# Performance work log

Hardware: AMD Instinct MI355X
Metric: run time of the kernel (lower is better)

Reference implementation:

```python
import jax, jax.numpy as jnp
import numpy as np

B, N, F, H, E = 2, 20000, 128, 1, 640000
C = F  # out_channels per head (concat=False -> mean over heads)
NEG_SLOPE = 0.2


def setup_inputs() -> dict:
    key = jax.random.key(0)
    k = jax.random.split(key, 6)
    x = jax.random.normal(k[0], (B, N, F), dtype=jnp.float32)
    edge_index = jax.random.randint(k[1], (2, E), 0, N, dtype=jnp.int64)
    s = 1.0 / np.sqrt(F)
    W = jax.random.normal(k[2], (H * C, F), dtype=jnp.float32) * s      # PyG Linear weight
    att_src = jax.random.normal(k[3], (H, C), dtype=jnp.float32) * s
    att_dst = jax.random.normal(k[4], (H, C), dtype=jnp.float32) * s
    bias = jnp.zeros((C,), dtype=jnp.float32)
    return {"x": x, "edge_index": edge_index, "W": W,
            "att_src": att_src, "att_dst": att_dst, "bias": bias}


def _gat_single(x, src, dst, W, att_src, att_dst, bias):
    # x: [N, F]; src/dst: [E'] (self-loops already appended)
    h = (x @ W.T).reshape(N, H, C)                      # [N, H, C]
    a_src = jnp.einsum('nhc,hc->nh', h, att_src)        # [N, H]
    a_dst = jnp.einsum('nhc,hc->nh', h, att_dst)        # [N, H]
    logits = jax.nn.leaky_relu(a_src[src] + a_dst[dst], NEG_SLOPE)  # [E', H]
    # edge-softmax over incoming edges of each dst node
    seg_max = jax.ops.segment_max(logits, dst, num_segments=N)      # [N, H]
    e = jnp.exp(logits - seg_max[dst])
    denom = jax.ops.segment_sum(e, dst, num_segments=N)             # [N, H]
    alpha = e / denom[dst]                                          # [E', H]
    msg = h[src] * alpha[:, :, None]                                # [E', H, C]
    out = jax.ops.segment_sum(msg, dst, num_segments=N)             # [N, H, C]
    return out.mean(axis=1) + bias                                  # [N, C]


def reference(x, edge_index, W, att_src, att_dst, bias):
    # PyG GATConv default: add self-loops
    loops = jnp.arange(N, dtype=edge_index.dtype)
    src = jnp.concatenate([edge_index[0], loops])
    dst = jnp.concatenate([edge_index[1], loops])
    f = lambda xb: _gat_single(xb, src, dst, W, att_src, att_dst, bias)
    return jax.vmap(f)(x)  # [B, N, F]
```

## Files before the change

### kernel.cpp

```cpp
#include <hip/hip_runtime.h>
#include <hip/hip_bf16.h>
#include <math.h>

#define BB    2
#define NN    20000
#define FF    128
#define EE    640000
#define NBIN  157
#define NBLK  625
#define SEGW  32
#define BSLOTS (NBLK * SEGW)
#define RECCAP 5120
#define GEMM_BLOCKS 625
#define SLOPE 0.2f

typedef __attribute__((ext_vector_type(8))) short bf16x8;
typedef __attribute__((ext_vector_type(4))) float f32x4;

static __device__ __forceinline__ ushort f2bf(float f) {
    unsigned u = __float_as_uint(f);
    u += 0x7fffu + ((u >> 16) & 1u);
    return (ushort)(u >> 16);
}
static __device__ __forceinline__ float bf2f(unsigned hw) {
    return __uint_as_float(hw << 16);
}
static __device__ __forceinline__ float bflo(unsigned q) {
    return __uint_as_float(q << 16);
}
static __device__ __forceinline__ float bfhi(unsigned q) {
    return __uint_as_float(q & 0xffff0000u);
}

__global__ __launch_bounds__(256) void fused_kernel(
    const float* __restrict__ x, const float* __restrict__ W,
    const float* __restrict__ att_src, const float* __restrict__ att_dst,
    const int* __restrict__ ei,
    unsigned* __restrict__ hbu, float* __restrict__ as2, float* __restrict__ ad2,
    ushort* __restrict__ cnts, unsigned* __restrict__ binbuf)
{
    __shared__ ushort XL[64 * 128];
    __shared__ ushort WL[128 * 128];
    const int tid = threadIdx.x;

    if (blockIdx.x >= GEMM_BLOCKS) {
        const int b2 = blockIdx.x - GEMM_BLOCKS;
        const int e0 = b2 * 1024;
        int* hcnt = (int*)XL;
        int* hofs = hcnt + 160;
        int* hcur = hofs + 160;
        int* scan = hcur + 160;
        unsigned* stage = (unsigned*)WL;

        for (int i = tid; i < NBIN; i += 256) { hcnt[i] = 0; hcur[i] = 0; }
        __syncthreads();

        int bin[4]; unsigned word[4];
        #pragma unroll
        for (int k = 0; k < 4; ++k) {
            int e = e0 + k * 256 + tid;
            int s = ei[e], d = ei[EE + e];
            bool ok = ((unsigned)s < NN) && ((unsigned)d < NN);
            bin[k] = ok ? (d >> 7) : -1;
            word[k] = ((unsigned)(d & 127) << 15) | (unsigned)(s & 0x7fff);
            if (ok) atomicAdd(&hcnt[bin[k]], 1);
        }
        __syncthreads();
        scan[tid] = (tid < NBIN) ? hcnt[tid] : 0;
        __syncthreads();
        #pragma unroll
        for (int o = 1; o < 256; o <<= 1) {
            int v = (tid >= o) ? scan[tid - o] : 0;
            __syncthreads();
            scan[tid] += v;
            __syncthreads();
        }
        if (tid < NBIN) hofs[tid] = scan[tid] - hcnt[tid];
        if (tid == 0) hofs[NBIN] = scan[NBIN - 1];
        if (tid < NBIN) cnts[b2 * NBIN + tid] = (ushort)min(hcnt[tid], SEGW);
        __syncthreads();
        #pragma unroll
        for (int k = 0; k < 4; ++k) {
            if (bin[k] >= 0) {
                int slot = atomicAdd(&hcur[bin[k]], 1);
                stage[hofs[bin[k]] + slot] = word[k];
            }
        }
        __syncthreads();
        const int total = hofs[NBIN];
        for (int i = tid; i < total; i += 256) {
            int lo = 0, hi = NBIN;
            while (hi - lo > 1) { int mid = (lo + hi) >> 1; if (hofs[mid] <= i) lo = mid; else hi = mid; }
            int j = i - hofs[lo];
            if (j < SEGW)
                binbuf[(size_t)lo * BSLOTS + b2 * SEGW + j] = stage[i];
        }
        return;
    }

    const int r0 = blockIdx.x * 64;
    {
        const float4* xg = (const float4*)(x + (size_t)r0 * 128);
        #pragma unroll
        for (int i = 0; i < 8; ++i) {
            int idx = tid + i * 256;
            int r = idx >> 5, k = (idx & 31) * 4;
            float4 v = xg[idx];
            ushort4 p = { f2bf(v.x), f2bf(v.y), f2bf(v.z), f2bf(v.w) };
            unsigned byte = ((unsigned)r << 8) + ((unsigned)k << 1);
            byte ^= (unsigned)(r & 7) << 4;
            *(ushort4*)((char*)XL + byte) = p;
        }
    }
    {
        const float4* wg = (const float4*)W;
        #pragma unroll
        for (int i = 0; i < 16; ++i) {
            int idx = tid + i * 256;
            int c = idx >> 5, k = (idx & 31) * 4;
            float4 v = wg[idx];
            ushort4 p = { f2bf(v.x), f2bf(v.y), f2bf(v.z), f2bf(v.w) };
            unsigned byte = ((unsigned)c << 8) + ((unsigned)k << 1);
            byte ^= (unsigned)(c & 7) << 4;
            *(ushort4*)((char*)WL + byte) = p;
        }
    }
    __syncthreads();

    const int wid = tid >> 6, lane = tid & 63;
    const int l15 = lane & 15, lg = lane >> 4;
    f32x4 acc[8];
    #pragma unroll
    for (int i = 0; i < 8; ++i) acc[i] = (f32x4){0.f, 0.f, 0.f, 0.f};

    const int arow = wid * 16 + l15;
    #pragma unroll
    for (int kt = 0; kt < 4; ++kt) {
        unsigned abyte = ((unsigned)arow << 8) + (unsigned)(kt * 64 + lg * 16);
        abyte ^= (unsigned)(arow & 7) << 4;
        bf16x8 af = *(const bf16x8*)((const char*)XL + abyte);
        #pragma unroll
        for (int ct = 0; ct < 8; ++ct) {
            int c = ct * 16 + l15;
            unsigned bbyte = ((unsigned)c << 8) + (unsigned)(kt * 64 + lg * 16);
            bbyte ^= (unsigned)(c & 7) << 4;
            bf16x8 bfr = *(const bf16x8*)((const char*)WL + bbyte);
            acc[ct] = __builtin_amdgcn_mfma_f32_16x16x32_bf16(af, bfr, acc[ct], 0, 0, 0);
        }
    }

    float ps0=0,ps1=0,ps2=0,ps3=0, pd0=0,pd1=0,pd2=0,pd3=0;
    #pragma unroll
    for (int ct = 0; ct < 8; ++ct) {
        int c = ct * 16 + l15;
        float as_ = att_src[c], ad_ = att_dst[c];
        ps0 += acc[ct][0]*as_; pd0 += acc[ct][0]*ad_;
        ps1 += acc[ct][1]*as_; pd1 += acc[ct][1]*ad_;
        ps2 += acc[ct][2]*as_; pd2 += acc[ct][2]*ad_;
        ps3 += acc[ct][3]*as_; pd3 += acc[ct][3]*ad_;
    }
    #pragma unroll
    for (int o = 1; o < 16; o <<= 1) {
        ps0 += __shfl_xor(ps0, o, 64); pd0 += __shfl_xor(pd0, o, 64);
        ps1 += __shfl_xor(ps1, o, 64); pd1 += __shfl_xor(pd1, o, 64);
        ps2 += __shfl_xor(ps2, o, 64); pd2 += __shfl_xor(pd2, o, 64);
        ps3 += __shfl_xor(ps3, o, 64); pd3 += __shfl_xor(pd3, o, 64);
    }
    if (l15 == 0) {
        int rb = r0 + wid * 16 + lg * 4;
        #pragma unroll
        for (int q = 0; q < 4; ++q) {
            int r = rb + q;
            int b = (r >= NN);
            int n = r - b * NN;
            float ps = q==0?ps0 : q==1?ps1 : q==2?ps2 : ps3;
            float pd = q==0?pd0 : q==1?pd1 : q==2?pd2 : pd3;
            as2[n * 2 + b] = ps;
            ad2[n * 2 + b] = pd;
        }
    }

    __syncthreads();
    ushort* hl = (ushort*)WL;
    {
        int rb = wid * 16 + lg * 4;
        #pragma unroll
        for (int ct = 0; ct < 8; ++ct) {
            int c = ct * 16 + l15;
            hl[(rb+0) * 128 + c] = f2bf(acc[ct][0]);
            hl[(rb+1) * 128 + c] = f2bf(acc[ct][1]);
            hl[(rb+2) * 128 + c] = f2bf(acc[ct][2]);
            hl[(rb+3) * 128 + c] = f2bf(acc[ct][3]);
        }
    }
    __syncthreads();
    {
        const unsigned* hs = (const unsigned*)hl;
        #pragma unroll
        for (int i = 0; i < 16; ++i) {
            int idx = tid + i * 256;
            int row = idx >> 6, p = idx & 63;
            int r = r0 + row;
            int b = (r >= NN);
            int n = r - b * NN;
            hbu[(size_t)n * 128 + p * 2 + b] = hs[row * 64 + p];
        }
    }
}

__global__ __launch_bounds__(1024) void sort_kernel(
    const ushort* __restrict__ cnts, const unsigned* __restrict__ binbuf,
    const float2* __restrict__ as2, const float2* __restrict__ ad2,
    uint2* __restrict__ rec, int* __restrict__ nodeStart,
    int* __restrict__ nodeCnt)
{
    __shared__ ushort cb[NBLK];
    __shared__ int ncnt[128];
    __shared__ int scan[128];
    __shared__ int nofs[128];
    __shared__ int ncur[128];
    const int b = blockIdx.x;
    const int tid = threadIdx.x;
    const unsigned* src = binbuf + (size_t)b * BSLOTS;

    for (int i = tid; i < NBLK; i += 1024) cb[i] = cnts[i * NBIN + b];
    if (tid < 128) {
        int n = b * 128 + tid;
        int self = (n < NN) ? 1 : 0;
        ncnt[tid] = self;
        ncur[tid] = self;
    }
    __syncthreads();
    for (int idx = tid; idx < BSLOTS; idx += 1024) {
        if ((idx & (SEGW - 1)) < cb[idx >> 5])
            atomicAdd(&ncnt[src[idx] >> 15], 1);
    }
    __syncthreads();
    if (tid < 128) scan[tid] = ncnt[tid];
    __syncthreads();
    #pragma unroll
    for (int o = 1; o < 128; o <<= 1) {
        int v = 0;
        if (tid < 128 && tid >= o) v = scan[tid - o];
        __syncthreads();
        if (tid < 128) scan[tid] += v;
        __syncthreads();
    }
    if (tid < 128) {
        nofs[tid] = scan[tid] - ncnt[tid];
        int n = b * 128 + tid;
        if (n < NN) {
            nodeStart[n] = b * RECCAP + nofs[tid];
            nodeCnt[n]   = ncnt[tid];
            float2 av = as2[n];
            float2 dv = ad2[n];
            float l0 = av.x + dv.x; l0 = l0 > 0.f ? l0 : SLOPE * l0;
            float l1 = av.y + dv.y; l1 = l1 > 0.f ? l1 : SLOPE * l1;
            int pos = nofs[tid];
            if (pos < RECCAP) {
                uint2 r = { (unsigned)n | ((unsigned)f2bf(__expf(l0)) << 16),
                            (unsigned)f2bf(__expf(l1)) };
                rec[(size_t)b * RECCAP + pos] = r;
            }
        }
    }
    __syncthreads();
    for (int idx = tid; idx < BSLOTS; idx += 1024) {
        if ((idx & (SEGW - 1)) < cb[idx >> 5]) {
            unsigned w = src[idx];
            int dl = w >> 15;
            int s  = w & 0x7fff;
            int d  = b * 128 + dl;
            float2 av = as2[s];
            float2 dv = ad2[d];
            float l0 = av.x + dv.x; l0 = l0 > 0.f ? l0 : SLOPE * l0;
            float l1 = av.y + dv.y; l1 = l1 > 0.f ? l1 : SLOPE * l1;
            int slot = atomicAdd(&ncur[dl], 1);
            int pos = nofs[dl] + slot;
            if (pos < RECCAP) {
                uint2 r = { (unsigned)s | ((unsigned)f2bf(__expf(l0)) << 16),
                            (unsigned)f2bf(__expf(l1)) };
                rec[(size_t)b * RECCAP + pos] = r;
            }
        }
    }
}

__global__ __launch_bounds__(256) void gather_kernel(
    const uint2* __restrict__ h,
    const int* __restrict__ nodeStart, const int* __restrict__ nodeCnt,
    const uint2* __restrict__ rec,
    const float* __restrict__ bias, float* __restrict__ out)
{
    const int tid = threadIdx.x;
    const int wid = tid >> 6, lane = tid & 63;
    const int n = blockIdx.x * 4 + wid;

    __shared__ ushort ssrc[4][128];
    __shared__ float2 swp[4][128];

    const int beg = nodeStart[n];
    const int cn = min(nodeCnt[n], 128);

    float den0 = 0.f, den1 = 0.f;
    #pragma unroll
    for (int r = 0; r < 2; ++r) {
        int j = r * 64 + lane;
        if (j < cn) {
            uint2 rc = rec[(size_t)beg + j];
            float w0 = bf2f(rc.x >> 16);
            float w1 = bf2f(rc.y & 0xffffu);
            ssrc[wid][j] = (ushort)(rc.x & 0xffffu);
            swp[wid][j] = (float2){w0, w1};
            den0 += w0; den1 += w1;
        }
    }
    #pragma unroll
    for (int o = 32; o > 0; o >>= 1) {
        den0 += __shfl_xor(den0, o, 64);
        den1 += __shfl_xor(den1, o, 64);
    }

    float a0x = 0.f, a0y = 0.f, a1x = 0.f, a1y = 0.f;
    int j = 0;
    for (; j + 3 < cn; j += 4) {
        int s0 = ssrc[wid][j],     s1 = ssrc[wid][j + 1];
        int s2 = ssrc[wid][j + 2], s3 = ssrc[wid][j + 3];
        uint2 q0 = h[(size_t)s0 * 64 + lane];
        uint2 q1 = h[(size_t)s1 * 64 + lane];
        uint2 q2 = h[(size_t)s2 * 64 + lane];
        uint2 q3 = h[(size_t)s3 * 64 + lane];
        float2 w0 = swp[wid][j],     w1 = swp[wid][j + 1];
        float2 w2 = swp[wid][j + 2], w3 = swp[wid][j + 3];
        a0x += w0.x * bflo(q0.x); a0y += w0.x * bfhi(q0.x);
        a1x += w0.y * bflo(q0.y); a1y += w0.y * bfhi(q0.y);
        a0x += w1.x * bflo(q1.x); a0y += w1.x * bfhi(q1.x);
        a1x += w1.y * bflo(q1.y); a1y += w1.y * bfhi(q1.y);
        a0x += w2.x * bflo(q2.x); a0y += w2.x * bfhi(q2.x);
        a1x += w2.y * bflo(q2.y); a1y += w2.y * bfhi(q2.y);
        a0x += w3.x * bflo(q3.x); a0y += w3.x * bfhi(q3.x);
        a1x += w3.y * bflo(q3.y); a1y += w3.y * bfhi(q3.y);
    }
    for (; j < cn; ++j) {
        int s0 = ssrc[wid][j];
        uint2 q0 = h[(size_t)s0 * 64 + lane];
        float2 w0 = swp[wid][j];
        a0x += w0.x * bflo(q0.x); a0y += w0.x * bfhi(q0.x);
        a1x += w0.y * bflo(q0.y); a1y += w0.y * bfhi(q0.y);
    }

    float r0 = 1.f / den0, r1 = 1.f / den1;
    float2 bv = *(const float2*)&bias[lane * 2];
    float2 o0 = { a0x * r0 + bv.x, a0y * r0 + bv.y };
    float2 o1 = { a1x * r1 + bv.x, a1y * r1 + bv.y };
    *(float2*)&out[(size_t)n * 128 + lane * 2]        = o0;
    *(float2*)&out[((size_t)NN + n) * 128 + lane * 2] = o1;
}

extern "C" void kernel_launch(void* const* d_in, const int* in_sizes, int n_in,
                              void* d_out, int out_size, void* d_ws, size_t ws_size,
                              hipStream_t stream)
{
    const float* x       = (const float*)d_in[0];
    const int*   ei      = (const int*)d_in[1];
    const float* W       = (const float*)d_in[2];
    const float* att_src = (const float*)d_in[3];
    const float* att_dst = (const float*)d_in[4];
    const float* bias    = (const float*)d_in[5];
    float* out = (float*)d_out;

    char* ws = (char*)d_ws;
    unsigned* hbu      = (unsigned*)(ws);
    float*    as2      = (float*)(ws + 10240000);
    float*    ad2      = (float*)(ws + 10400000);
    ushort*   cnts     = (ushort*)(ws + 10560000);
    unsigned* binbuf   = (unsigned*)(ws + 10756352);
    uint2*    rec      = (uint2*)(ws + 23316352);
    int*      nodeStart= (int*)(ws + 29747072);
    int*      nodeCnt  = (int*)(ws + 29827072);

    fused_kernel<<<GEMM_BLOCKS + NBLK, 256, 0, stream>>>(
        x, W, att_src, att_dst, ei, hbu, as2, ad2, cnts, binbuf);
    sort_kernel<<<NBIN, 1024, 0, stream>>>(cnts, binbuf,
                                           (const float2*)as2, (const float2*)ad2,
                                           rec, nodeStart, nodeCnt);
    gather_kernel<<<NN / 4, 256, 0, stream>>>((const uint2*)hbu, nodeStart,
                                              nodeCnt, rec, bias, out);
}
```

Measured before the change: 79.64 us.

## Split gather across feature quarters with four nodes per wavefront

The gather kernel now splits the 128 feature channels into four 32-channel slices across blocks. Each wavefront handles four destination nodes with 16 lanes each, instead of one node per 64-lane wavefront. Each slice-group of blocks reads only its own quarter of h, which may improve cache locality and give more independent nodes per wave. In exchange, every edge record is re-read and the softmax denominator recomputed four times. Lanes also idle while waiting for the longest of the four nodes in their wave (cnmax), and the unroll drops from 4 to 2.

```diff
diff --git a/kernel.cpp b/kernel.cpp
--- a/kernel.cpp
+++ b/kernel.cpp
@@ -294,67 +294,68 @@
 {
     const int tid = threadIdx.x;
     const int wid = tid >> 6, lane = tid & 63;
-    const int n = blockIdx.x * 4 + wid;
-
-    __shared__ ushort ssrc[4][128];
-    __shared__ float2 swp[4][128];
+    const int sub = lane >> 4, pp = lane & 15;
+    const int q = blockIdx.x / 1250;
+    const int g = blockIdx.x - q * 1250;
+    const int n = g * 16 + wid * 4 + sub;
+
+    __shared__ ushort ssrc[4][4][128];
+    __shared__ float2 swp[4][4][128];
 
     const int beg = nodeStart[n];
     const int cn = min(nodeCnt[n], 128);
 
     float den0 = 0.f, den1 = 0.f;
-    #pragma unroll
-    for (int r = 0; r < 2; ++r) {
-        int j = r * 64 + lane;
-        if (j < cn) {
-            uint2 rc = rec[(size_t)beg + j];
-            float w0 = bf2f(rc.x >> 16);
-            float w1 = bf2f(rc.y & 0xffffu);
-            ssrc[wid][j] = (ushort)(rc.x & 0xffffu);
-            swp[wid][j] = (float2){w0, w1};
-            den0 += w0; den1 += w1;
-        }
-    }
-    #pragma unroll
-    for (int o = 32; o > 0; o >>= 1) {
+    for (int j = pp; j < cn; j += 16) {
+        uint2 rc = rec[(size_t)beg + j];
+        float w0 = bf2f(rc.x >> 16);
+        float w1 = bf2f(rc.y & 0xffffu);
+        ssrc[wid][sub][j] = (ushort)(rc.x & 0xffffu);
+        swp[wid][sub][j] = (float2){w0, w1};
+        den0 += w0; den1 += w1;
+    }
+    #pragma unroll
+    for (int o = 1; o < 16; o <<= 1) {
         den0 += __shfl_xor(den0, o, 64);
         den1 += __shfl_xor(den1, o, 64);
     }
 
+    int cnmax = cn;
+    cnmax = max(cnmax, __shfl_xor(cnmax, 16, 64));
+    cnmax = max(cnmax, __shfl_xor(cnmax, 32, 64));
+
+    const uint2* hq = h + q * 16;
     float a0x = 0.f, a0y = 0.f, a1x = 0.f, a1y = 0.f;
     int j = 0;
-    for (; j + 3 < cn; j += 4) {
-        int s0 = ssrc[wid][j],     s1 = ssrc[wid][j + 1];
-        int s2 = ssrc[wid][j + 2], s3 = ssrc[wid][j + 3];
-        uint2 q0 = h[(size_t)s0 * 64 + lane];
-        uint2 q1 = h[(size_t)s1 * 64 + lane];
-        uint2 q2 = h[(size_t)s2 * 64 + lane];
-        uint2 q3 = h[(size_t)s3 * 64 + lane];
-        float2 w0 = swp[wid][j],     w1 = swp[wid][j + 1];
-        float2 w2 = swp[wid][j + 2], w3 = swp[wid][j + 3];
+    for (; j + 1 < cnmax; j += 2) {
+        bool v0 = (j < cn), v1 = (j + 1 < cn);
+        int s0 = v0 ? ssrc[wid][sub][j]     : 0;
+        int s1 = v1 ? ssrc[wid][sub][j + 1] : 0;
+        uint2 q0 = hq[(size_t)s0 * 64 + pp];
+        uint2 q1 = hq[(size_t)s1 * 64 + pp];
+        float2 w0 = v0 ? swp[wid][sub][j]     : (float2){0.f, 0.f};
+        float2 w1 = v1 ? swp[wid][sub][j + 1] : (float2){0.f, 0.f};
         a0x += w0.x * bflo(q0.x); a0y += w0.x * bfhi(q0.x);
         a1x += w0.y * bflo(q0.y); a1y += w0.y * bfhi(q0.y);
         a0x += w1.x * bflo(q1.x); a0y += w1.x * bfhi(q1.x);
         a1x += w1.y * bflo(q1.y); a1y += w1.y * bfhi(q1.y);
-        a0x += w2.x * bflo(q2.x); a0y += w2.x * bfhi(q2.x);
-        a1x += w2.y * bflo(q2.y); a1y += w2.y * bfhi(q2.y);
-        a0x += w3.x * bflo(q3.x); a0y += w3.x * bfhi(q3.x);
-        a1x += w3.y * bflo(q3.y); a1y += w3.y * bfhi(q3.y);
-    }
-    for (; j < cn; ++j) {
-        int s0 = ssrc[wid][j];
-        uint2 q0 = h[(size_t)s0 * 64 + lane];
-        float2 w0 = swp[wid][j];
+    }
+    if (j < cnmax) {
+        bool v0 = (j < cn);
+        int s0 = v0 ? ssrc[wid][sub][j] : 0;
+        uint2 q0 = hq[(size_t)s0 * 64 + pp];
+        float2 w0 = v0 ? swp[wid][sub][j] : (float2){0.f, 0.f};
         a0x += w0.x * bflo(q0.x); a0y += w0.x * bfhi(q0.x);
         a1x += w0.y * bflo(q0.y); a1y += w0.y * bfhi(q0.y);
     }
 
     float r0 = 1.f / den0, r1 = 1.f / den1;
-    float2 bv = *(const float2*)&bias[lane * 2];
+    int c0 = q * 32 + pp * 2;
+    float2 bv = *(const float2*)&bias[c0];
     float2 o0 = { a0x * r0 + bv.x, a0y * r0 + bv.y };
     float2 o1 = { a1x * r1 + bv.x, a1y * r1 + bv.y };
-    *(float2*)&out[(size_t)n * 128 + lane * 2]        = o0;
-    *(float2*)&out[((size_t)NN + n) * 128 + lane * 2] = o1;
+    *(float2*)&out[(size_t)n * 128 + c0]        = o0;
+    *(float2*)&out[((size_t)NN + n) * 128 + c0] = o1;
 }
 
 extern "C" void kernel_launch(void* const* d_in, const int* in_sizes, int n_in,
@@ -384,6 +385,6 @@
     sort_kernel<<<NBIN, 1024, 0, stream>>>(cnts, binbuf,
                                            (const float2*)as2, (const float2*)ad2,
                                            rec, nodeStart, nodeCnt);
-    gather_kernel<<<NN / 4, 256, 0, stream>>>((const uint2*)hbu, nodeStart,
-                                              nodeCnt, rec, bias, out);
-}
+    gather_kernel<<<4 * 1250, 256, 0, stream>>>((const uint2*)hbu, nodeStart,
+                                                nodeCnt, rec, bias, out);
+}
```

New measurement: 80.86 us. Within noise of the previous version (+1.5%).
